# Kernel optimization log

Hardware: AMD Instinct MI355X
Metric: run time of the kernel (lower is better)

## Reference

```python
import jax, jax.numpy as jnp
import numpy as np

D_K = 512  # attn_dim

def setup_inputs() -> dict:
    key = jax.random.key(0)
    ks = jax.random.split(key, 10)
    B, S, D, A, Dv = 8, 2048, 1024, 512, 512
    Q = jax.random.normal(ks[0], (B, S, D), dtype=jnp.float32)
    K = jax.random.normal(ks[1], (B, S, D), dtype=jnp.float32)
    V = jax.random.normal(ks[2], (B, S, D), dtype=jnp.float32)
    attn_mask = jax.random.randint(ks[3], (B, S, S), 0, 2, dtype=jnp.int32)
    s = 1.0 / np.sqrt(D)
    Wq = jax.random.normal(ks[4], (A, D), dtype=jnp.float32) * s
    bq = jnp.zeros((A,), dtype=jnp.float32)
    Wk = jax.random.normal(ks[5], (A, D), dtype=jnp.float32) * s
    bk = jnp.zeros((A,), dtype=jnp.float32)
    Wv = jax.random.normal(ks[6], (Dv, D), dtype=jnp.float32) * s
    bv = jnp.zeros((Dv,), dtype=jnp.float32)
    return {"Q": Q, "K": K, "V": V, "attn_mask": attn_mask,
            "Wq": Wq, "bq": bq, "Wk": Wk, "bk": bk, "Wv": Wv, "bv": bv}

def reference(Q, K, V, attn_mask, Wq, bq, Wk, bk, Wv, bv):
    # Linear projections (torch Linear: x @ W.T + b)
    Qp = jnp.einsum('bsd,ad->bsa', Q, Wq) + bq          # [B,S,A]
    Kp = jnp.einsum('bsd,ad->bsa', K, Wk) + bk          # [B,S,A]
    WV = jnp.einsum('bsd,vd->bsv', V, Wv) + bv          # [B,S,Dv]
    scale = 1.0 / np.sqrt(D_K).astype(np.float32)
    scores = jnp.einsum('bqa,bka->bqk', Qp, Kp) * scale  # [B,S,S]
    scores = scores + attn_mask.astype(scores.dtype) * (-1e9)
    scores = jnp.swapaxes(scores, -1, -2)               # transpose BEFORE softmax
    attn = jax.nn.softmax(scores, axis=-1)              # normalize over query axis
    selfOutput = jnp.einsum('bkq,bqv->bkv', attn, WV)   # [B,S,Dv]
    return selfOutput, attn
```

## Files before the change

kernel.cpp:

```cpp
#include <hip/hip_runtime.h>
#include <stdint.h>

#define B_N   8
#define S_N   2048
#define D_N   1024
#define A_N   512
#define DV_N  512

typedef __attribute__((ext_vector_type(8))) short bf16x8;
typedef __attribute__((ext_vector_type(4))) float f32x4;

__device__ __forceinline__ unsigned short f2bf(float x) {
    union { float f; unsigned int u; } v; v.f = x;
    return (unsigned short)((v.u + 0x7fffu + ((v.u >> 16) & 1u)) >> 16);
}

__global__ void cvt_f32_bf16(const float* __restrict__ src,
                             unsigned short* __restrict__ dst, int n4) {
    int i = blockIdx.x * blockDim.x + threadIdx.x;
    if (i >= n4) return;
    float4 v = ((const float4*)src)[i];
    ushort4 o;
    o.x = f2bf(v.x); o.y = f2bf(v.y); o.z = f2bf(v.z); o.w = f2bf(v.w);
    ((ushort4*)dst)[i] = o;
}

__device__ __forceinline__ void gld_lds16(const void* g, void* l) {
    __builtin_amdgcn_global_load_lds(
        (const __attribute__((address_space(1))) unsigned int*)g,
        (__attribute__((address_space(3))) unsigned int*)l, 16, 0, 0);
}

template <int MODE>
__global__ __launch_bounds__(256) void gemm_nt(
    const unsigned short* __restrict__ A, const unsigned short* __restrict__ B,
    void* __restrict__ C, const float* __restrict__ bias,
    const int* __restrict__ mask, int M, int N, int K,
    long long sA, long long sB, long long sC, float scale)
{
    __shared__ __align__(16) unsigned short As[128 * 32];
    __shared__ __align__(16) unsigned short Bs[128 * 32];

    const int tid  = threadIdx.x;
    const int wave = tid >> 6;
    const int lane = tid & 63;
    const int lrow = lane & 15;
    const int quad = lane >> 4;
    const int wm = wave & 1;
    const int wn = wave >> 1;
    const int b  = blockIdx.z;
    const int m0 = blockIdx.y * 128;
    const int n0 = blockIdx.x * 128;

    const unsigned short* Ab = A + (long long)b * sA;
    const unsigned short* Bb = B + (long long)b * sB;

    f32x4 acc[4][4];
#pragma unroll
    for (int i = 0; i < 4; ++i)
#pragma unroll
        for (int j = 0; j < 4; ++j) acc[i][j] = (f32x4){0.f, 0.f, 0.f, 0.f};

    const int srow = lane >> 2;
    const int scol = (lane & 3) * 8;

    for (int kt = 0; kt < K; kt += 32) {
#pragma unroll
        for (int t = 0; t < 2; ++t) {
            const int seg = t * 4 + wave;
            const unsigned short* ga =
                Ab + (long long)(m0 + seg * 16 + srow) * K + kt + scol;
            gld_lds16(ga, &As[seg * 16 * 32]);
            const unsigned short* gb =
                Bb + (long long)(n0 + seg * 16 + srow) * K + kt + scol;
            gld_lds16(gb, &Bs[seg * 16 * 32]);
        }
        __syncthreads();

        bf16x8 af[4], bfr[4];
#pragma unroll
        for (int i = 0; i < 4; ++i)
            af[i] = *(const bf16x8*)&As[(wm * 64 + i * 16 + lrow) * 32 + quad * 8];
#pragma unroll
        for (int j = 0; j < 4; ++j)
            bfr[j] = *(const bf16x8*)&Bs[(wn * 64 + j * 16 + lrow) * 32 + quad * 8];
#pragma unroll
        for (int i = 0; i < 4; ++i)
#pragma unroll
            for (int j = 0; j < 4; ++j)
                acc[i][j] = __builtin_amdgcn_mfma_f32_16x16x32_bf16(
                    af[i], bfr[j], acc[i][j], 0, 0, 0);
        __syncthreads();
    }

#pragma unroll
    for (int i = 0; i < 4; ++i) {
        const int rowb = m0 + wm * 64 + i * 16 + quad * 4;
#pragma unroll
        for (int j = 0; j < 4; ++j) {
            const int col = n0 + wn * 64 + j * 16 + lrow;
#pragma unroll
            for (int r = 0; r < 4; ++r) {
                const int row = rowb + r;
                float v = acc[i][j][r];
                if (MODE == 0) {
                    v += bias[col];
                    ((unsigned short*)C)[(long long)row * N + col] = f2bf(v);
                } else if (MODE == 1) {
                    v += bias[row];
                    (((unsigned short*)C) + (long long)b * sC)
                        [(long long)row * N + col] = f2bf(v);
                } else if (MODE == 2) {
                    v *= scale;
                    const int mv = mask[(long long)b * S_N * S_N +
                                        (long long)col * S_N + row];
                    v += (float)mv * -1e9f;
                    (((float*)C) + (long long)b * sC)[(long long)row * N + col] = v;
                } else {
                    (((float*)C) + (long long)b * sC)[(long long)row * N + col] = v;
                }
            }
        }
    }
}

__global__ __launch_bounds__(256) void softmax_rows(
    float* __restrict__ sT, unsigned short* __restrict__ pbf)
{
    const long long row = blockIdx.x;
    float* p = sT + row * S_N;
    unsigned short* q = pbf + row * S_N;
    const int tid = threadIdx.x;
    const int wave = tid >> 6, lane = tid & 63;

    float4 v0 = ((const float4*)p)[tid];
    float4 v1 = ((const float4*)p)[tid + 256];

    float mx = fmaxf(fmaxf(fmaxf(v0.x, v0.y), fmaxf(v0.z, v0.w)),
                     fmaxf(fmaxf(v1.x, v1.y), fmaxf(v1.z, v1.w)));
#pragma unroll
    for (int off = 32; off; off >>= 1) mx = fmaxf(mx, __shfl_xor(mx, off));

    __shared__ float redm[4];
    __shared__ float reds[4];
    if (lane == 0) redm[wave] = mx;
    __syncthreads();
    mx = fmaxf(fmaxf(redm[0], redm[1]), fmaxf(redm[2], redm[3]));

    float e[8];
    e[0] = __expf(v0.x - mx); e[1] = __expf(v0.y - mx);
    e[2] = __expf(v0.z - mx); e[3] = __expf(v0.w - mx);
    e[4] = __expf(v1.x - mx); e[5] = __expf(v1.y - mx);
    e[6] = __expf(v1.z - mx); e[7] = __expf(v1.w - mx);

    float sum = e[0] + e[1] + e[2] + e[3] + e[4] + e[5] + e[6] + e[7];
#pragma unroll
    for (int off = 32; off; off >>= 1) sum += __shfl_xor(sum, off);
    if (lane == 0) reds[wave] = sum;
    __syncthreads();
    sum = reds[0] + reds[1] + reds[2] + reds[3];
    const float inv = 1.0f / sum;

    float4 o0 = {e[0] * inv, e[1] * inv, e[2] * inv, e[3] * inv};
    float4 o1 = {e[4] * inv, e[5] * inv, e[6] * inv, e[7] * inv};
    ((float4*)p)[tid]       = o0;
    ((float4*)p)[tid + 256] = o1;
    ushort4 b0 = {f2bf(o0.x), f2bf(o0.y), f2bf(o0.z), f2bf(o0.w)};
    ushort4 b1 = {f2bf(o1.x), f2bf(o1.y), f2bf(o1.z), f2bf(o1.w)};
    ((ushort4*)q)[tid]       = b0;
    ((ushort4*)q)[tid + 256] = b1;
}

extern "C" void kernel_launch(void* const* d_in, const int* in_sizes, int n_in,
                              void* d_out, int out_size, void* d_ws, size_t ws_size,
                              hipStream_t stream) {
    const float* Q    = (const float*)d_in[0];
    const float* K    = (const float*)d_in[1];
    const float* V    = (const float*)d_in[2];
    const int*   mask = (const int*)d_in[3];
    const float* Wq   = (const float*)d_in[4];
    const float* bq   = (const float*)d_in[5];
    const float* Wk   = (const float*)d_in[6];
    const float* bk   = (const float*)d_in[7];
    const float* Wv   = (const float*)d_in[8];
    const float* bv   = (const float*)d_in[9];

    float* out      = (float*)d_out;
    float* attn_out = out + (long long)B_N * S_N * DV_N;

    unsigned short* Qbf  = (unsigned short*)d_ws;
    unsigned short* Kbf  = Qbf + (long long)B_N * S_N * D_N;
    unsigned short* attn_bf = Qbf;
    unsigned short* Vbf  = Kbf + (long long)B_N * S_N * D_N;
    unsigned short* Wqbf = Vbf + (long long)B_N * S_N * D_N;
    unsigned short* Wkbf = Wqbf + (long long)A_N * D_N;
    unsigned short* Wvbf = Wkbf + (long long)A_N * D_N;
    unsigned short* Qp   = Wvbf + (long long)DV_N * D_N;
    unsigned short* Kp   = Qp + (long long)B_N * S_N * A_N;
    unsigned short* WVt  = Kp + (long long)B_N * S_N * A_N;

    const float scale = 0.044194173824159216f;

    {
        long long nQ = (long long)B_N * S_N * D_N;
        long long nW = (long long)A_N * D_N;
        int n4;
        n4 = (int)(nQ / 4);
        cvt_f32_bf16<<<dim3((n4 + 255) / 256), dim3(256), 0, stream>>>(Q, Qbf, n4);
        cvt_f32_bf16<<<dim3((n4 + 255) / 256), dim3(256), 0, stream>>>(K, Kbf, n4);
        cvt_f32_bf16<<<dim3((n4 + 255) / 256), dim3(256), 0, stream>>>(V, Vbf, n4);
        n4 = (int)(nW / 4);
        cvt_f32_bf16<<<dim3((n4 + 255) / 256), dim3(256), 0, stream>>>(Wq, Wqbf, n4);
        cvt_f32_bf16<<<dim3((n4 + 255) / 256), dim3(256), 0, stream>>>(Wk, Wkbf, n4);
        cvt_f32_bf16<<<dim3((n4 + 255) / 256), dim3(256), 0, stream>>>(Wv, Wvbf, n4);
    }

    gemm_nt<0><<<dim3(A_N / 128, (B_N * S_N) / 128, 1), dim3(256), 0, stream>>>(
        Qbf, Wqbf, (void*)Qp, bq, nullptr, B_N * S_N, A_N, D_N, 0, 0, 0, 1.0f);
    gemm_nt<0><<<dim3(A_N / 128, (B_N * S_N) / 128, 1), dim3(256), 0, stream>>>(
        Kbf, Wkbf, (void*)Kp, bk, nullptr, B_N * S_N, A_N, D_N, 0, 0, 0, 1.0f);
    gemm_nt<1><<<dim3(S_N / 128, DV_N / 128, B_N), dim3(256), 0, stream>>>(
        Wvbf, Vbf, (void*)WVt, bv, nullptr, DV_N, S_N, D_N,
        0, (long long)S_N * D_N, (long long)DV_N * S_N, 1.0f);
    gemm_nt<2><<<dim3(S_N / 128, S_N / 128, B_N), dim3(256), 0, stream>>>(
        Kp, Qp, (void*)attn_out, nullptr, mask, S_N, S_N, A_N,
        (long long)S_N * A_N, (long long)S_N * A_N, (long long)S_N * S_N, scale);
    softmax_rows<<<dim3(B_N * S_N), dim3(256), 0, stream>>>(attn_out, attn_bf);
    gemm_nt<3><<<dim3(DV_N / 128, S_N / 128, B_N), dim3(256), 0, stream>>>(
        attn_bf, WVt, (void*)out, nullptr, nullptr, S_N, DV_N, S_N,
        (long long)S_N * S_N, (long long)DV_N * S_N, (long long)S_N * DV_N, 1.0f);
}
```

Measured before the change: 690.4 us.

## Pack mask into transposed bitmask and apply it in softmax instead of GEMM epilogue

Adds a kernel that reads the int32 mask coalesced, transposes it through shared memory, and packs it into bits via wave ballots. The scores GEMM no longer does a strided per-element mask gather in its epilogue; softmax applies the -1e9 bias from the compact bitmask instead. This removes uncoalesced mask traffic at the cost of an extra kernel launch and a small workspace buffer.

New measurement: 686.6 us. Within noise of the previous version (-0.6%).

```diff
diff --git a/kernel.cpp b/kernel.cpp
--- a/kernel.cpp
+++ b/kernel.cpp
@@ -31,11 +31,43 @@
         (__attribute__((address_space(3))) unsigned int*)l, 16, 0, 0);
 }
 
+__global__ __launch_bounds__(256) void pack_maskT(const int* __restrict__ mask,
+                                                  unsigned int* __restrict__ mpT) {
+    __shared__ int tile[64 * 129];
+    const int b  = blockIdx.z;
+    const int q0 = blockIdx.y * 64;
+    const int k0 = blockIdx.x * 128;
+    const int tid = threadIdx.x;
+    const long long base = (long long)b * S_N * S_N;
+#pragma unroll
+    for (int it = 0; it < 8; ++it) {
+        int c = it * 256 + tid;
+        int row  = c >> 5;
+        int col4 = (c & 31) * 4;
+        int4 v = *(const int4*)&mask[base + (long long)(q0 + row) * S_N + k0 + col4];
+        int* d = &tile[row * 129 + col4];
+        d[0] = v.x; d[1] = v.y; d[2] = v.z; d[3] = v.w;
+    }
+    __syncthreads();
+    const int wave = tid >> 6, lane = tid & 63;
+#pragma unroll
+    for (int kk = 0; kk < 32; ++kk) {
+        const int k = wave * 32 + kk;
+        const int v = tile[lane * 129 + k];
+        const unsigned long long bal = __ballot(v != 0);
+        if (lane == 0) {
+            unsigned int* o = &mpT[(long long)(b * S_N + k0 + k) * 64 + (q0 >> 5)];
+            o[0] = (unsigned int)bal;
+            o[1] = (unsigned int)(bal >> 32);
+        }
+    }
+}
+
 template <int MODE>
 __global__ __launch_bounds__(256) void gemm_nt(
     const unsigned short* __restrict__ A, const unsigned short* __restrict__ B,
     void* __restrict__ C, const float* __restrict__ bias,
-    const int* __restrict__ mask, int M, int N, int K,
+    int M, int N, int K,
     long long sA, long long sB, long long sC, float scale)
 {
     __shared__ __align__(16) unsigned short As[128 * 32];
@@ -112,9 +144,6 @@
                         [(long long)row * N + col] = f2bf(v);
                 } else if (MODE == 2) {
                     v *= scale;
-                    const int mv = mask[(long long)b * S_N * S_N +
-                                        (long long)col * S_N + row];
-                    v += (float)mv * -1e9f;
                     (((float*)C) + (long long)b * sC)[(long long)row * N + col] = v;
                 } else {
                     (((float*)C) + (long long)b * sC)[(long long)row * N + col] = v;
@@ -125,7 +154,8 @@
 }
 
 __global__ __launch_bounds__(256) void softmax_rows(
-    float* __restrict__ sT, unsigned short* __restrict__ pbf)
+    float* __restrict__ sT, unsigned short* __restrict__ pbf,
+    const unsigned int* __restrict__ mpT)
 {
     const long long row = blockIdx.x;
     float* p = sT + row * S_N;
@@ -135,6 +165,19 @@
 
     float4 v0 = ((const float4*)p)[tid];
     float4 v1 = ((const float4*)p)[tid + 256];
+
+    const unsigned int* mp = mpT + row * 64;
+    const unsigned int w0 = mp[tid >> 3];
+    const unsigned int w1 = mp[32 + (tid >> 3)];
+    const int sh = (tid & 7) * 4;
+    v0.x += ((w0 >> (sh + 0)) & 1u) ? -1e9f : 0.0f;
+    v0.y += ((w0 >> (sh + 1)) & 1u) ? -1e9f : 0.0f;
+    v0.z += ((w0 >> (sh + 2)) & 1u) ? -1e9f : 0.0f;
+    v0.w += ((w0 >> (sh + 3)) & 1u) ? -1e9f : 0.0f;
+    v1.x += ((w1 >> (sh + 0)) & 1u) ? -1e9f : 0.0f;
+    v1.y += ((w1 >> (sh + 1)) & 1u) ? -1e9f : 0.0f;
+    v1.z += ((w1 >> (sh + 2)) & 1u) ? -1e9f : 0.0f;
+    v1.w += ((w1 >> (sh + 3)) & 1u) ? -1e9f : 0.0f;
 
     float mx = fmaxf(fmaxf(fmaxf(v0.x, v0.y), fmaxf(v0.z, v0.w)),
                      fmaxf(fmaxf(v1.x, v1.y), fmaxf(v1.z, v1.w)));
@@ -198,8 +241,11 @@
     unsigned short* Qp   = Wvbf + (long long)DV_N * D_N;
     unsigned short* Kp   = Qp + (long long)B_N * S_N * A_N;
     unsigned short* WVt  = Kp + (long long)B_N * S_N * A_N;
+    unsigned int*   mpT  = (unsigned int*)(WVt + (long long)B_N * DV_N * S_N);
 
     const float scale = 0.044194173824159216f;
+
+    pack_maskT<<<dim3(S_N / 128, S_N / 64, B_N), dim3(256), 0, stream>>>(mask, mpT);
 
     {
         long long nQ = (long long)B_N * S_N * D_N;
@@ -216,17 +262,17 @@
     }
 
     gemm_nt<0><<<dim3(A_N / 128, (B_N * S_N) / 128, 1), dim3(256), 0, stream>>>(
-        Qbf, Wqbf, (void*)Qp, bq, nullptr, B_N * S_N, A_N, D_N, 0, 0, 0, 1.0f);
+        Qbf, Wqbf, (void*)Qp, bq, B_N * S_N, A_N, D_N, 0, 0, 0, 1.0f);
     gemm_nt<0><<<dim3(A_N / 128, (B_N * S_N) / 128, 1), dim3(256), 0, stream>>>(
-        Kbf, Wkbf, (void*)Kp, bk, nullptr, B_N * S_N, A_N, D_N, 0, 0, 0, 1.0f);
+        Kbf, Wkbf, (void*)Kp, bk, B_N * S_N, A_N, D_N, 0, 0, 0, 1.0f);
     gemm_nt<1><<<dim3(S_N / 128, DV_N / 128, B_N), dim3(256), 0, stream>>>(
-        Wvbf, Vbf, (void*)WVt, bv, nullptr, DV_N, S_N, D_N,
+        Wvbf, Vbf, (void*)WVt, bv, DV_N, S_N, D_N,
         0, (long long)S_N * D_N, (long long)DV_N * S_N, 1.0f);
     gemm_nt<2><<<dim3(S_N / 128, S_N / 128, B_N), dim3(256), 0, stream>>>(
-        Kp, Qp, (void*)attn_out, nullptr, mask, S_N, S_N, A_N,
+        Kp, Qp, (void*)attn_out, nullptr, S_N, S_N, A_N,
         (long long)S_N * A_N, (long long)S_N * A_N, (long long)S_N * S_N, scale);
-    softmax_rows<<<dim3(B_N * S_N), dim3(256), 0, stream>>>(attn_out, attn_bf);
+    softmax_rows<<<dim3(B_N * S_N), dim3(256), 0, stream>>>(attn_out, attn_bf, mpT);
     gemm_nt<3><<<dim3(DV_N / 128, S_N / 128, B_N), dim3(256), 0, stream>>>(
-        attn_bf, WVt, (void*)out, nullptr, nullptr, S_N, DV_N, S_N,
+        attn_bf, WVt, (void*)out, nullptr, S_N, DV_N, S_N,
         (long long)S_N * S_N, (long long)DV_N * S_N, (long long)S_N * DV_N, 1.0f);
 }
```
